# Performance work log

Measured on AMD Instinct MI355X. Metric: run time of the kernel, lower is better.

The kernel has to match this reference:

```python
import jax, jax.numpy as jnp
import numpy as np

D = 256
H1, H2 = 256, 128

def setup_inputs() -> dict:
    key0 = jax.random.key(0)
    ks = jax.random.split(key0, 10)
    B, Lq, Lk = 2, 512, 512
    query = jax.random.normal(ks[0], (B, Lq, D), dtype=jnp.float32)
    key_t = jax.random.normal(ks[1], (B, Lk, D), dtype=jnp.float32)
    value = jax.random.normal(ks[2], (B, Lk, D), dtype=jnp.float32)
    mask = jnp.ones((B, Lq, Lk), dtype=jnp.int32)
    s1 = 1.0 / np.sqrt(2 * D)
    W1 = jax.random.uniform(ks[3], (2 * D, H1), jnp.float32, -s1, s1)  # torch Linear(2D,H1), [in,out]
    b1 = jax.random.uniform(ks[4], (H1,), jnp.float32, -s1, s1)
    s2 = 1.0 / np.sqrt(H1)
    W2 = jax.random.uniform(ks[5], (H1, H2), jnp.float32, -s2, s2)
    b2 = jax.random.uniform(ks[6], (H2,), jnp.float32, -s2, s2)
    s3 = 1.0 / np.sqrt(H2)
    W3 = jax.random.uniform(ks[7], (H2, 1), jnp.float32, -s3, s3)
    b3 = jax.random.uniform(ks[8], (1,), jnp.float32, -s3, s3)
    return {"query": query, "key": key_t, "value": value, "mask": mask,
            "W1": W1, "b1": b1, "W2": W2, "b2": b2, "W3": W3, "b3": b3}

def reference(query, key, value, mask, W1, b1, W2, b2, W3, b3):
    # Original: cat([q_i, k_j]) @ W1 == q_i @ W1[:D] + k_j @ W1[D:]  (algebraic split,
    # identical math, avoids materializing the [B,Lq,Lk,2D] concat tensor).
    W1q, W1k = W1[:D], W1[D:]
    qp = jnp.einsum('bqd,dh->bqh', query, W1q)           # [B,Lq,H1]
    kp = jnp.einsum('bkd,dh->bkh', key, W1k)             # [B,Lk,H1]
    h1 = jax.nn.relu(qp[:, :, None, :] + kp[:, None, :, :] + b1)   # [B,Lq,Lk,H1]
    h2 = jax.nn.relu(jnp.einsum('bqkh,hj->bqkj', h1, W2) + b2)      # [B,Lq,Lk,H2]
    scores = (jnp.einsum('bqkj,jo->bqko', h2, W3) + b3)[..., 0]     # [B,Lq,Lk]
    scores = jnp.where(mask == 0, jnp.float32(-1e9), scores)
    attn = jax.nn.softmax(scores, axis=-1)               # dropout is identity in eval mode
    out = jnp.einsum('bqk,bkd->bqd', attn, value)
    return out, attn
```

## Files before the change

kernel.cpp:

```cpp
#include <hip/hip_runtime.h>

#define D_  256
#define H1_ 256
#define H2_ 128
#define B_  2
#define LQ_ 512
#define LK_ 512
#define BK  64

typedef float  f32x4  __attribute__((ext_vector_type(4)));
typedef __bf16 bf16x8 __attribute__((ext_vector_type(8)));
typedef __bf16 bf16x4 __attribute__((ext_vector_type(4)));

__global__ __launch_bounds__(512) void prep_kernel(
    const float* __restrict__ query, const float* __restrict__ key,
    const float* __restrict__ W1, const float* __restrict__ b1,
    const float* __restrict__ W2,
    float* __restrict__ qp, float* __restrict__ kp, __bf16* __restrict__ w2f) {
  const int blk = blockIdx.x;
  const int tid = threadIdx.x;
  if (blk >= 512) {
    const int id   = (blk - 512) * 512 + tid;
    const int j    = id & 7;
    const int lane = (id >> 3) & 63;
    const int frag = id >> 9;
    const int nt = frag & 3;
    const int wn = (frag >> 2) & 1;
    const int ks = (frag >> 3) & 1;
    const int kc = frag >> 4;
    const int n = wn * 64 + nt * 16 + (lane & 15);
    const int k = kc * 64 + ks * 32 + ((lane >> 4) << 3) + j;
    w2f[id] = (__bf16)W2[k * H2_ + n];
    return;
  }
  __shared__ float in_lds[4][D_];
  __shared__ float part[4][H1_];
  const int row0 = blk * 4;
  const int sel  = row0 >> 10;
  const float* __restrict__ src = sel ? key : query;
  const int base = (row0 & 1023) * D_;
  for (int i = tid; i < 4 * D_; i += 512)
    in_lds[i >> 8][i & 255] = src[base + i];
  __syncthreads();
  const int h  = tid & 255;
  const int kh = tid >> 8;
  float acc[4] = {0.f, 0.f, 0.f, 0.f};
  const float* __restrict__ w = W1 + sel * D_ * H1_ + kh * 128 * H1_ + h;
#pragma unroll 4
  for (int dd = 0; dd < 128; ++dd) {
    const float wv = w[dd * H1_];
    const int d = kh * 128 + dd;
#pragma unroll
    for (int r = 0; r < 4; ++r) acc[r] += in_lds[r][d] * wv;
  }
  if (kh == 1) {
#pragma unroll
    for (int r = 0; r < 4; ++r) part[r][h] = acc[r];
  }
  __syncthreads();
  if (kh == 0) {
    const float bias = sel ? 0.0f : b1[h];
    float* __restrict__ dst = sel ? kp : qp;
#pragma unroll
    for (int r = 0; r < 4; ++r)
      dst[base + r * H1_ + h] = acc[r] + part[r][h] + bias;
  }
}

__global__ __launch_bounds__(512, 2) void score_kernel(
    const float* __restrict__ qp, const float* __restrict__ kp,
    const __bf16* __restrict__ w2f,
    const float* __restrict__ b2, const float* __restrict__ W3,
    const float* __restrict__ b3, float* __restrict__ scores) {
  __shared__ __align__(16) __bf16 A_lds[256 * BK];
  __shared__ float  spart[2][256];

  const int b  = blockIdx.z;
  const int q0 = blockIdx.y * 8;
  const int k0 = blockIdx.x * 32;
  const int tid  = threadIdx.x;
  const int wave = tid >> 6;
  const int lane = tid & 63;
  const int quad = lane >> 4;
  const int l16  = lane & 15;
  const int wm   = wave >> 1;
  const int wn   = wave & 1;
  const int h8   = l16 & 7;

  const int qi   = wave;
  const int kseg = (tid >> 4) & 3;
  const int kg   = tid & 15;

  const float* __restrict__ qpb = qp + (b * LQ_ + q0) * H1_;
  const float* __restrict__ kpb = kp + (b * LK_ + k0) * H1_;

  f32x4 acc[4][4];
#pragma unroll
  for (int mt = 0; mt < 4; ++mt)
#pragma unroll
    for (int nt = 0; nt < 4; ++nt)
      acc[mt][nt] = (f32x4){0.f, 0.f, 0.f, 0.f};

  for (int kc = 0; kc < H1_ / BK; ++kc) {
    bf16x8 bfr[2][4];
#pragma unroll
    for (int ks = 0; ks < 2; ++ks)
#pragma unroll
      for (int nt = 0; nt < 4; ++nt)
        bfr[ks][nt] = *(const bf16x8*)(
            w2f + ((((kc * 2 + ks) * 2 + wn) * 4 + nt) * 64 + lane) * 8);

    const float4 qv = *(const float4*)(qpb + qi * H1_ + kc * BK + kg * 4);
#pragma unroll
    for (int ii = 0; ii < 8; ++ii) {
      const int ki = kseg * 8 + ii;
      const int r  = qi * 32 + ki;
      const float4 kv = *(const float4*)(kpb + ki * H1_ + kc * BK + kg * 4);
      bf16x4 a;
      a[0] = (__bf16)fmaxf(qv.x + kv.x, 0.f);
      a[1] = (__bf16)fmaxf(qv.y + kv.y, 0.f);
      a[2] = (__bf16)fmaxf(qv.z + kv.z, 0.f);
      a[3] = (__bf16)fmaxf(qv.w + kv.w, 0.f);
      const int sw = (((kg >> 1) ^ (r & 7)) << 3) + ((kg & 1) << 2);
      *(bf16x4*)(&A_lds[r * BK + sw]) = a;
    }
    __syncthreads();
#pragma unroll
    for (int ks = 0; ks < 2; ++ks) {
      const int cbase = ks * 4 + quad;
      bf16x8 af[4];
#pragma unroll
      for (int mt = 0; mt < 4; ++mt) {
        const int ra = wm * 64 + mt * 16 + l16;
        af[mt] = *(const bf16x8*)(&A_lds[ra * BK + ((cbase ^ h8) << 3)]);
      }
#pragma unroll
      for (int mt = 0; mt < 4; ++mt)
#pragma unroll
        for (int nt = 0; nt < 4; ++nt)
          acc[mt][nt] = __builtin_amdgcn_mfma_f32_16x16x32_bf16(
              af[mt], bfr[ks][nt], acc[mt][nt], 0, 0, 0);
    }
    __syncthreads();
  }

  float part[4][4];
#pragma unroll
  for (int mt = 0; mt < 4; ++mt)
#pragma unroll
    for (int rg = 0; rg < 4; ++rg) part[mt][rg] = 0.f;
#pragma unroll
  for (int nt = 0; nt < 4; ++nt) {
    const int col = wn * 64 + nt * 16 + l16;
    const float b2v = b2[col];
    const float w3v = W3[col];
#pragma unroll
    for (int mt = 0; mt < 4; ++mt)
#pragma unroll
      for (int rg = 0; rg < 4; ++rg) {
        float h2 = acc[mt][nt][rg] + b2v;
        h2 = fmaxf(h2, 0.f);
        part[mt][rg] += h2 * w3v;
      }
  }
#pragma unroll
  for (int off = 1; off < 16; off <<= 1)
#pragma unroll
    for (int mt = 0; mt < 4; ++mt)
#pragma unroll
      for (int rg = 0; rg < 4; ++rg)
        part[mt][rg] += __shfl_xor(part[mt][rg], off, 64);
  if (l16 == 0) {
#pragma unroll
    for (int mt = 0; mt < 4; ++mt)
#pragma unroll
      for (int rg = 0; rg < 4; ++rg) {
        const int rl = wm * 64 + mt * 16 + quad * 4 + rg;
        spart[wn][rl] = part[mt][rg];
      }
  }
  __syncthreads();
  if (tid < 256) {
    const float s = spart[0][tid] + spart[1][tid] + b3[0];
    const int qi2 = tid >> 5, ki2 = tid & 31;
    scores[(b * LQ_ + q0 + qi2) * LK_ + k0 + ki2] = s;
  }
}

__global__ __launch_bounds__(512) void smout_kernel(
    const float* __restrict__ sc, float* __restrict__ attn,
    const int* __restrict__ mask, const float* __restrict__ value,
    float* __restrict__ out) {
  const int ds = blockIdx.x, qg = blockIdx.y, b = blockIdx.z;
  const int tid = threadIdx.x;
  __shared__ __align__(16) float a_lds[LK_][4];
  __shared__ float p_lds[3][4][128];
  const int row0 = b * LQ_ + qg * 4;
  const int w = tid >> 6, lane = tid & 63;
  if (w < 4) {
    const float* __restrict__ srow = sc + (row0 + w) * LK_;
    const int*  __restrict__ mrow = mask + (row0 + w) * LK_;
    float v[8];
#pragma unroll
    for (int j = 0; j < 8; ++j) {
      float s = srow[lane + j * 64];
      if (mrow[lane + j * 64] == 0) s = -1e9f;
      v[j] = s;
    }
    float m = v[0];
#pragma unroll
    for (int j = 1; j < 8; ++j) m = fmaxf(m, v[j]);
#pragma unroll
    for (int off = 32; off; off >>= 1) m = fmaxf(m, __shfl_xor(m, off, 64));
    float sum = 0.f;
#pragma unroll
    for (int j = 0; j < 8; ++j) { v[j] = __expf(v[j] - m); sum += v[j]; }
#pragma unroll
    for (int off = 32; off; off >>= 1) sum += __shfl_xor(sum, off, 64);
    const float inv = 1.f / sum;
    float* __restrict__ arow = attn + (row0 + w) * LK_;
#pragma unroll
    for (int j = 0; j < 8; ++j) {
      const float p = v[j] * inv;
      a_lds[lane + j * 64][w] = p;
      if (ds == 0) arow[lane + j * 64] = p;
    }
  }
  __syncthreads();
  const int dl = tid & 127;
  const int d  = dl + ds * 128;
  const int kh = tid >> 7;
  float acc[4] = {0.f, 0.f, 0.f, 0.f};
  const float* __restrict__ vb = value + (b * LK_ + kh * 128) * D_ + d;
#pragma unroll 4
  for (int k = 0; k < 128; ++k) {
    const float v = vb[k * D_];
    const f32x4 pv = *(const f32x4*)(&a_lds[kh * 128 + k][0]);
#pragma unroll
    for (int q = 0; q < 4; ++q) acc[q] += pv[q] * v;
  }
  if (kh > 0) {
#pragma unroll
    for (int q = 0; q < 4; ++q) p_lds[kh - 1][q][dl] = acc[q];
  }
  __syncthreads();
  if (kh == 0) {
    float* __restrict__ ob = out + row0 * D_ + d;
#pragma unroll
    for (int q = 0; q < 4; ++q)
      ob[q * D_] = acc[q] + p_lds[0][q][dl] + p_lds[1][q][dl] + p_lds[2][q][dl];
  }
}

extern "C" void kernel_launch(void* const* d_in, const int* in_sizes, int n_in,
                              void* d_out, int out_size, void* d_ws, size_t ws_size,
                              hipStream_t stream) {
  (void)in_sizes; (void)n_in; (void)out_size; (void)ws_size;
  const float* query = (const float*)d_in[0];
  const float* key   = (const float*)d_in[1];
  const float* value = (const float*)d_in[2];
  const int*   mask  = (const int*)d_in[3];
  const float* W1    = (const float*)d_in[4];
  const float* b1    = (const float*)d_in[5];
  const float* W2    = (const float*)d_in[6];
  const float* b2    = (const float*)d_in[7];
  const float* W3    = (const float*)d_in[8];
  const float* b3    = (const float*)d_in[9];

  float* out  = (float*)d_out;
  float* attn = out + B_ * LQ_ * D_;

  float*  qp  = (float*)d_ws;
  float*  kp  = qp + B_ * LQ_ * H1_;
  __bf16* w2f = (__bf16*)(kp + B_ * LK_ * H1_);
  float*  sc  = (float*)(w2f + H2_ * H1_);

  prep_kernel<<<576, 512, 0, stream>>>(query, key, W1, b1, W2, qp, kp, w2f);
  dim3 gscore(LK_ / 32, LQ_ / 8, B_);
  score_kernel<<<gscore, 512, 0, stream>>>(qp, kp, w2f, b2, W3, b3, sc);
  smout_kernel<<<dim3(2, 128, B_), 512, 0, stream>>>(sc, attn, mask, value, out);
}
```

Measured before the change: 164.4 us.

## Build MFMA A-fragments in registers directly, dropping LDS staging in score kernel

The score kernel now forms each lane's relu(qp+kp) bf16 A-fragment straight from global memory into registers, laid out to match the MFMA operand, instead of writing it to a swizzled LDS tile and reading it back. This removes the LDS round trip and the two barriers per K-chunk. Blocks shrink to 256 threads covering 8 queries by 16 keys, so the grid doubles. The cost is redundant global/L2 loads of qp and kp rows across lanes and waves, plus more W2 fragment reloads per output, since each block now covers fewer keys.

```diff
diff --git a/kernel.cpp b/kernel.cpp
--- a/kernel.cpp
+++ b/kernel.cpp
@@ -67,17 +67,16 @@
   }
 }
 
-__global__ __launch_bounds__(512, 2) void score_kernel(
+__global__ __launch_bounds__(256) void score_kernel(
     const float* __restrict__ qp, const float* __restrict__ kp,
     const __bf16* __restrict__ w2f,
     const float* __restrict__ b2, const float* __restrict__ W3,
     const float* __restrict__ b3, float* __restrict__ scores) {
-  __shared__ __align__(16) __bf16 A_lds[256 * BK];
-  __shared__ float  spart[2][256];
+  __shared__ float spart[2][128];
 
   const int b  = blockIdx.z;
   const int q0 = blockIdx.y * 8;
-  const int k0 = blockIdx.x * 32;
+  const int k0 = blockIdx.x * 16;
   const int tid  = threadIdx.x;
   const int wave = tid >> 6;
   const int lane = tid & 63;
@@ -85,14 +84,12 @@
   const int l16  = lane & 15;
   const int wm   = wave >> 1;
   const int wn   = wave & 1;
-  const int h8   = l16 & 7;
-
-  const int qi   = wave;
-  const int kseg = (tid >> 4) & 3;
-  const int kg   = tid & 15;
 
   const float* __restrict__ qpb = qp + (b * LQ_ + q0) * H1_;
   const float* __restrict__ kpb = kp + (b * LK_ + k0) * H1_;
+  const float* __restrict__ krow = kpb + l16 * H1_ + quad * 8;
+  const float* __restrict__ qrow = qpb + (wm * 4) * H1_ + quad * 8;
+  const __bf16* __restrict__ wb  = w2f + (wn * 4 * 64 + lane) * 8;
 
   f32x4 acc[4][4];
 #pragma unroll
@@ -101,47 +98,38 @@
     for (int nt = 0; nt < 4; ++nt)
       acc[mt][nt] = (f32x4){0.f, 0.f, 0.f, 0.f};
 
-  for (int kc = 0; kc < H1_ / BK; ++kc) {
-    bf16x8 bfr[2][4];
-#pragma unroll
-    for (int ks = 0; ks < 2; ++ks)
+#pragma unroll
+  for (int kc = 0; kc < 4; ++kc) {
+#pragma unroll
+    for (int ks = 0; ks < 2; ++ks) {
+      const int ko = kc * 64 + ks * 32;
+      bf16x8 bfr[4];
 #pragma unroll
       for (int nt = 0; nt < 4; ++nt)
-        bfr[ks][nt] = *(const bf16x8*)(
-            w2f + ((((kc * 2 + ks) * 2 + wn) * 4 + nt) * 64 + lane) * 8);
-
-    const float4 qv = *(const float4*)(qpb + qi * H1_ + kc * BK + kg * 4);
-#pragma unroll
-    for (int ii = 0; ii < 8; ++ii) {
-      const int ki = kseg * 8 + ii;
-      const int r  = qi * 32 + ki;
-      const float4 kv = *(const float4*)(kpb + ki * H1_ + kc * BK + kg * 4);
-      bf16x4 a;
-      a[0] = (__bf16)fmaxf(qv.x + kv.x, 0.f);
-      a[1] = (__bf16)fmaxf(qv.y + kv.y, 0.f);
-      a[2] = (__bf16)fmaxf(qv.z + kv.z, 0.f);
-      a[3] = (__bf16)fmaxf(qv.w + kv.w, 0.f);
-      const int sw = (((kg >> 1) ^ (r & 7)) << 3) + ((kg & 1) << 2);
-      *(bf16x4*)(&A_lds[r * BK + sw]) = a;
-    }
-    __syncthreads();
-#pragma unroll
-    for (int ks = 0; ks < 2; ++ks) {
-      const int cbase = ks * 4 + quad;
+        bfr[nt] = *(const bf16x8*)(wb + ((kc * 2 + ks) * 8 + nt) * 512);
+      const float4 kv0 = *(const float4*)(krow + ko);
+      const float4 kv1 = *(const float4*)(krow + ko + 4);
       bf16x8 af[4];
 #pragma unroll
       for (int mt = 0; mt < 4; ++mt) {
-        const int ra = wm * 64 + mt * 16 + l16;
-        af[mt] = *(const bf16x8*)(&A_lds[ra * BK + ((cbase ^ h8) << 3)]);
+        const float4 qv0 = *(const float4*)(qrow + mt * H1_ + ko);
+        const float4 qv1 = *(const float4*)(qrow + mt * H1_ + ko + 4);
+        af[mt][0] = (__bf16)fmaxf(qv0.x + kv0.x, 0.f);
+        af[mt][1] = (__bf16)fmaxf(qv0.y + kv0.y, 0.f);
+        af[mt][2] = (__bf16)fmaxf(qv0.z + kv0.z, 0.f);
+        af[mt][3] = (__bf16)fmaxf(qv0.w + kv0.w, 0.f);
+        af[mt][4] = (__bf16)fmaxf(qv1.x + kv1.x, 0.f);
+        af[mt][5] = (__bf16)fmaxf(qv1.y + kv1.y, 0.f);
+        af[mt][6] = (__bf16)fmaxf(qv1.z + kv1.z, 0.f);
+        af[mt][7] = (__bf16)fmaxf(qv1.w + kv1.w, 0.f);
       }
 #pragma unroll
       for (int mt = 0; mt < 4; ++mt)
 #pragma unroll
         for (int nt = 0; nt < 4; ++nt)
           acc[mt][nt] = __builtin_amdgcn_mfma_f32_16x16x32_bf16(
-              af[mt], bfr[ks][nt], acc[mt][nt], 0, 0, 0);
+              af[mt], bfr[nt], acc[mt][nt], 0, 0, 0);
     }
-    __syncthreads();
   }
 
   float part[4][4];
@@ -180,9 +168,9 @@
       }
   }
   __syncthreads();
-  if (tid < 256) {
+  if (tid < 128) {
     const float s = spart[0][tid] + spart[1][tid] + b3[0];
-    const int qi2 = tid >> 5, ki2 = tid & 31;
+    const int qi2 = tid >> 4, ki2 = tid & 15;
     scores[(b * LQ_ + q0 + qi2) * LK_ + k0 + ki2] = s;
   }
 }
@@ -276,7 +264,7 @@
   float*  sc  = (float*)(w2f + H2_ * H1_);
 
   prep_kernel<<<576, 512, 0, stream>>>(query, key, W1, b1, W2, qp, kp, w2f);
-  dim3 gscore(LK_ / 32, LQ_ / 8, B_);
-  score_kernel<<<gscore, 512, 0, stream>>>(qp, kp, w2f, b2, W3, b3, sc);
+  dim3 gscore(LK_ / 16, LQ_ / 8, B_);
+  score_kernel<<<gscore, 256, 0, stream>>>(qp, kp, w2f, b2, W3, b3, sc);
   smout_kernel<<<dim3(2, 128, B_), 512, 0, stream>>>(sc, attn, mask, value, out);
 }
```

Measured after the change: 181.2 us. 1.1x slower.
